# Kernel tuning notes

Hardware: AMD Instinct MI355X
Metric: run time of the kernel (lower is better)

## Reference

```python
import jax, jax.numpy as jnp
import numpy as np

N_NODES = 50000
N_EDGES = 800000
N_FEATS = 64
K_HOPS = 3


def setup_inputs() -> dict:
    key = jax.random.key(0)
    k1, k2, k3 = jax.random.split(key, 3)
    x = jax.random.normal(k1, (N_NODES, N_FEATS), dtype=jnp.float32)
    edge_index = jax.random.randint(k2, (2, N_EDGES), 0, N_NODES, dtype=jnp.int32)
    # SGConv linear: out_channels = 1 (hardcoded in Net)
    W = jax.random.normal(k3, (1, N_FEATS), dtype=jnp.float32) / np.sqrt(N_FEATS)
    b = jnp.zeros((1,), dtype=jnp.float32)
    return {"x": x, "edge_index": edge_index, "W": W, "b": b}


def reference(x, edge_index, W, b):
    # SGConv: X' = (D^-1/2 (A + I) D^-1/2)^K X @ W.T + b
    N = x.shape[0]
    self_loops = jnp.arange(N, dtype=edge_index.dtype)
    row = jnp.concatenate([edge_index[0], self_loops])  # source nodes (x_j)
    col = jnp.concatenate([edge_index[1], self_loops])  # destination nodes
    # gcn_norm: degree computed at destination with unit edge weights
    deg = jax.ops.segment_sum(jnp.ones(row.shape[0], x.dtype), col, num_segments=N)
    dinv = jnp.where(deg > 0, jax.lax.rsqrt(deg), jnp.zeros_like(deg))
    norm = dinv[row] * dinv[col]  # [E + N]
    # K hops of normalized sparse propagation: out[col] += norm * x[row]
    for _ in range(K_HOPS):
        x = jax.ops.segment_sum(norm[:, None] * x[row], col, num_segments=N)
    return x @ W.T + b  # [N, 1]
```

## Files before the change

kernel.cpp:

```cpp
#include <hip/hip_runtime.h>

#define N_NODES 50000
#define N_EDGES 800000
#define N_FEATS 64
#define EB4     (N_EDGES / 4)
#define NBUCK   256
#define BRANGE  196
#define CAPB    4096
#define NTHR    1024
#define CHUNK   ((EB4 + NBUCK - 1) / NBUCK)
#define MAXREC  (CHUNK * 4)

union SmemU {
    struct { unsigned buf[MAXREC]; unsigned adr[MAXREC]; } so;
    unsigned recs_l[CAPB];
};

__device__ __forceinline__ void gbar(unsigned* bar, unsigned target) {
    __syncthreads();
    if (threadIdx.x == 0) {
        __hip_atomic_fetch_add(bar, 1u, __ATOMIC_RELAXED, __HIP_MEMORY_SCOPE_AGENT);
        while (__hip_atomic_load(bar, __ATOMIC_RELAXED, __HIP_MEMORY_SCOPE_AGENT) < target)
            __builtin_amdgcn_s_sleep(2);
    }
    __syncthreads();
}

__device__ __forceinline__ void st_agent(float* p, float v) {
    __hip_atomic_store(p, v, __ATOMIC_RELAXED, __HIP_MEMORY_SCOPE_AGENT);
}
__device__ __forceinline__ void st_agent_u(unsigned* p, unsigned v) {
    __hip_atomic_store(p, v, __ATOMIC_RELAXED, __HIP_MEMORY_SCOPE_AGENT);
}
__device__ __forceinline__ float ld_agent(const float* p) {
    return __hip_atomic_load(p, __ATOMIC_RELAXED, __HIP_MEMORY_SCOPE_AGENT);
}
__device__ __forceinline__ unsigned ld_agent_u(const unsigned* p) {
    return __hip_atomic_load(p, __ATOMIC_RELAXED, __HIP_MEMORY_SCOPE_AGENT);
}
__device__ __forceinline__ unsigned long long ld_agent_u64(const unsigned long long* p) {
    return __hip_atomic_load(p, __ATOMIC_RELAXED, __HIP_MEMORY_SCOPE_AGENT);
}

__global__ void __launch_bounds__(NTHR) k_fused(
    const float* __restrict__ x, const int* __restrict__ ei,
    const float* __restrict__ w, const float* __restrict__ bptr,
    float* __restrict__ out,
    unsigned* __restrict__ bars, int* __restrict__ gcur,
    unsigned* __restrict__ recs, float* __restrict__ z0, float* __restrict__ z1)
{
    __shared__ SmemU u;
    __shared__ int   s_cnt[NBUCK];
    __shared__ int   s_off[NBUCK];
    __shared__ int   s_wsum[4];
    __shared__ int   s_total;
    __shared__ float s_dinv[BRANGE];
    __shared__ float s_z[BRANGE];
    __shared__ float s_acc[BRANGE];

    const int t = threadIdx.x;
    const int blk = blockIdx.x;
    const int* row = ei;
    const int* col = ei + N_EDGES;

    if (t < NBUCK) s_cnt[t] = 0;
    __syncthreads();

    const int g = blk * CHUNK + t;
    const bool valid = (t < CHUNK) && (g < EB4);
    int4 c4, r4;
    int bk0, bk1, bk2, bk3, rk0, rk1, rk2, rk3;
    if (valid) {
        c4 = ((const int4*)col)[g];
        r4 = ((const int4*)row)[g];
        bk0 = c4.x / BRANGE; rk0 = atomicAdd(&s_cnt[bk0], 1);
        bk1 = c4.y / BRANGE; rk1 = atomicAdd(&s_cnt[bk1], 1);
        bk2 = c4.z / BRANGE; rk2 = atomicAdd(&s_cnt[bk2], 1);
        bk3 = c4.w / BRANGE; rk3 = atomicAdd(&s_cnt[bk3], 1);
    }
    __syncthreads();

    if (t < NBUCK) {
        const int lane = t & 63;
        const int cnt = s_cnt[t];
        int val = cnt;
        #pragma unroll
        for (int d = 1; d < 64; d <<= 1) {
            int tmp = __shfl_up(val, d);
            if (lane >= d) val += tmp;
        }
        if (lane == 63) s_wsum[t >> 6] = val;
        s_off[t] = val - cnt;
    }
    __syncthreads();
    if (t < NBUCK) {
        const int w4 = t >> 6;
        int base = 0;
        #pragma unroll
        for (int i = 0; i < 3; i++) if (i < w4) base += s_wsum[i];
        s_off[t] += base;
        const int cnt = s_cnt[t];
        s_cnt[t] = cnt ? atomicAdd(&gcur[t], cnt) : 0;
        if (t == 0) s_total = s_wsum[0] + s_wsum[1] + s_wsum[2] + s_wsum[3];
    }
    __syncthreads();

    if (valid) {
        const int cc[4] = {c4.x, c4.y, c4.z, c4.w};
        const int rr[4] = {r4.x, r4.y, r4.z, r4.w};
        const int bb[4] = {bk0, bk1, bk2, bk3};
        const int kk[4] = {rk0, rk1, rk2, rk3};
        #pragma unroll
        for (int i = 0; i < 4; i++) {
            const int b = bb[i];
            const int p = s_off[b] + kk[i];
            const int slot = s_cnt[b] + kk[i];
            u.so.buf[p] = ((unsigned)(cc[i] - b * BRANGE) << 16) | (unsigned)rr[i];
            u.so.adr[p] = (slot < CAPB) ? (unsigned)(b * CAPB + slot) : 0xFFFFFFFFu;
        }
    }
    __syncthreads();

    const int total = s_total;
    for (int p = t; p < total; p += NTHR) {
        const unsigned a = u.so.adr[p];
        if (a != 0xFFFFFFFFu) st_agent_u(&recs[a], u.so.buf[p]);
    }

    const int ln = t >> 2;
    const int pp = t & 3;
    const int node = blk * BRANGE + ln;
    if (ln < BRANGE && node < N_NODES) {
        const float4* xr = (const float4*)(x + (size_t)node * N_FEATS + pp * 16);
        const float4* wr = (const float4*)(w + pp * 16);
        float a = 0.0f;
        #pragma unroll
        for (int k = 0; k < 4; k++) {
            const float4 v = xr[k];
            const float4 q = wr[k];
            a += v.x * q.x + v.y * q.y + v.z * q.z + v.w * q.w;
        }
        a += __shfl_xor(a, 1);
        a += __shfl_xor(a, 2);
        if (pp == 0) s_z[ln] = a;
    }
    __syncthreads();
    if (t < BRANGE) s_cnt[t] = 0;

    gbar(bars, 1 * NBUCK);

    const int sz = min((int)ld_agent_u((const unsigned*)&gcur[blk]), CAPB);

    const unsigned long long* rb2 =
        (const unsigned long long*)(recs + (size_t)blk * CAPB);
    const int sz2 = sz >> 1;
    for (int e = t; e < sz2; e += NTHR) {
        const unsigned long long v = ld_agent_u64(&rb2[e]);
        const unsigned r0 = (unsigned)v;
        const unsigned r1 = (unsigned)(v >> 32);
        ((unsigned long long*)u.recs_l)[e] = v;
        atomicAdd(&s_cnt[r0 >> 16], 1);
        atomicAdd(&s_cnt[r1 >> 16], 1);
    }
    if (t == 0 && (sz & 1)) {
        const unsigned r = ld_agent_u(&recs[(size_t)blk * CAPB + sz - 1]);
        u.recs_l[sz - 1] = r;
        atomicAdd(&s_cnt[r >> 16], 1);
    }
    __syncthreads();

    if (t < BRANGE) {
        const float d = rsqrtf((float)(s_cnt[t] + 1));
        s_dinv[t] = d;
        const int nd = blk * BRANGE + t;
        if (nd < N_NODES) {
            const float zv = d * s_z[t];
            s_z[t] = zv;
            st_agent(&z0[nd], zv);
        }
    }

    gbar(bars, 2 * NBUCK);

    const float* zin = z0;
    float* zout = z1;
    const int sz4 = sz >> 2;
    #pragma unroll 1
    for (int hop = 0; hop < 3; ++hop) {
        if (t < BRANGE) s_acc[t] = 0.0f;
        __syncthreads();

        const uint4* rl4 = (const uint4*)u.recs_l;
        for (int e = t; e < sz4; e += NTHR) {
            const uint4 r = rl4[e];
            const float v0 = ld_agent(&zin[r.x & 0xFFFFu]);
            const float v1 = ld_agent(&zin[r.y & 0xFFFFu]);
            const float v2 = ld_agent(&zin[r.z & 0xFFFFu]);
            const float v3 = ld_agent(&zin[r.w & 0xFFFFu]);
            atomicAdd(&s_acc[r.x >> 16], v0);
            atomicAdd(&s_acc[r.y >> 16], v1);
            atomicAdd(&s_acc[r.z >> 16], v2);
            atomicAdd(&s_acc[r.w >> 16], v3);
        }
        if (t < (sz & 3)) {
            const unsigned r = u.recs_l[(sz4 << 2) + t];
            atomicAdd(&s_acc[r >> 16], ld_agent(&zin[r & 0xFFFFu]));
        }
        __syncthreads();

        if (t < BRANGE) {
            const int nd = blk * BRANGE + t;
            if (nd < N_NODES) {
                const float d = s_dinv[t];
                const float v = s_z[t] + s_acc[t];
                if (hop == 2) {
                    out[nd] = d * v + bptr[0];
                } else {
                    const float nz = d * d * v;
                    s_z[t] = nz;
                    st_agent(&zout[nd], nz);
                }
            }
        }
        if (hop < 2) {
            gbar(bars, (unsigned)(3 + hop) * NBUCK);
            const float* tmp = zin;
            zin = zout;
            zout = const_cast<float*>(tmp);
        }
    }
}


extern "C" void kernel_launch(void* const* d_in, const int* in_sizes, int n_in,
                              void* d_out, int out_size, void* d_ws, size_t ws_size,
                              hipStream_t stream) {
    const float* x  = (const float*)d_in[0];
    const int*   ei = (const int*)d_in[1];
    const float* W  = (const float*)d_in[2];
    const float* b  = (const float*)d_in[3];
    float* out = (float*)d_out;

    unsigned* bars = (unsigned*)d_ws;
    int*      gcur = (int*)(bars + 64);
    unsigned* recs = (unsigned*)(gcur + NBUCK);
    float*    z0   = (float*)(recs + (size_t)NBUCK * CAPB);
    float*    z1   = z0 + N_NODES;

    hipMemsetAsync(bars, 0, (64 + NBUCK) * sizeof(unsigned), stream);

    k_fused<<<dim3(NBUCK), dim3(NTHR), 0, stream>>>(
        x, ei, W, b, out, bars, gcur, recs, z0, z1);
}
```

Measured before the change: 115.9 us.

## Shard grid barrier counters, triple-buffer z, and use plain cached gather loads

Replaces the single-counter grid barrier with 32 sharded counters that are polled by a warp and summed with shuffles, which cuts atomic contention on one address. It uses three separate z buffers (one per hop) so the gathers can use plain cached loads instead of agent-scope atomic loads. The z arrays get a padded per-block stride, with source indices remapped at record build time. The x·W projection is moved earlier so it overlaps the bucketing, and record loading is unrolled into two loads per thread. The risk is that plain loads of freshly written z values depend on caches staying coherent across the barrier, since each hop writes to a fresh buffer.

```diff
diff --git a/kernel.cpp b/kernel.cpp
--- a/kernel.cpp
+++ b/kernel.cpp
@@ -6,40 +6,72 @@
 #define EB4     (N_EDGES / 4)
 #define NBUCK   256
 #define BRANGE  196
+#define ZSTRIDE 208
 #define CAPB    4096
 #define NTHR    1024
 #define CHUNK   ((EB4 + NBUCK - 1) / NBUCK)
 #define MAXREC  (CHUNK * 4)
+#define BARW    32
 
 union SmemU {
     struct { unsigned buf[MAXREC]; unsigned adr[MAXREC]; } so;
     unsigned recs_l[CAPB];
 };
 
-__device__ __forceinline__ void gbar(unsigned* bar, unsigned target) {
-    __syncthreads();
-    if (threadIdx.x == 0) {
-        __hip_atomic_fetch_add(bar, 1u, __ATOMIC_RELAXED, __HIP_MEMORY_SCOPE_AGENT);
-        while (__hip_atomic_load(bar, __ATOMIC_RELAXED, __HIP_MEMORY_SCOPE_AGENT) < target)
-            __builtin_amdgcn_s_sleep(2);
-    }
-    __syncthreads();
-}
-
 __device__ __forceinline__ void st_agent(float* p, float v) {
     __hip_atomic_store(p, v, __ATOMIC_RELAXED, __HIP_MEMORY_SCOPE_AGENT);
 }
 __device__ __forceinline__ void st_agent_u(unsigned* p, unsigned v) {
     __hip_atomic_store(p, v, __ATOMIC_RELAXED, __HIP_MEMORY_SCOPE_AGENT);
 }
-__device__ __forceinline__ float ld_agent(const float* p) {
-    return __hip_atomic_load(p, __ATOMIC_RELAXED, __HIP_MEMORY_SCOPE_AGENT);
-}
 __device__ __forceinline__ unsigned ld_agent_u(const unsigned* p) {
     return __hip_atomic_load(p, __ATOMIC_RELAXED, __HIP_MEMORY_SCOPE_AGENT);
 }
 __device__ __forceinline__ unsigned long long ld_agent_u64(const unsigned long long* p) {
     return __hip_atomic_load(p, __ATOMIC_RELAXED, __HIP_MEMORY_SCOPE_AGENT);
+}
+
+__device__ __forceinline__ void gbar(unsigned* bars, int k) {
+    __syncthreads();
+    const int t = threadIdx.x;
+    if (t == 0)
+        __hip_atomic_fetch_add(&bars[k * BARW + (blockIdx.x & (BARW - 1))], 1u,
+                               __ATOMIC_RELAXED, __HIP_MEMORY_SCOPE_AGENT);
+    if (t < BARW) {
+        unsigned s;
+        do {
+            __builtin_amdgcn_s_sleep(1);
+            s = __hip_atomic_load(&bars[k * BARW + t],
+                                  __ATOMIC_RELAXED, __HIP_MEMORY_SCOPE_AGENT);
+            #pragma unroll
+            for (int d = 1; d < BARW; d <<= 1)
+                s += (unsigned)__shfl_xor((int)s, d);
+        } while (s < NBUCK);
+    }
+    __syncthreads();
+}
+
+__device__ __forceinline__ void gather(const unsigned* recs_l, int sz,
+                                       const float* __restrict__ zin,
+                                       float* s_acc) {
+    const int t = threadIdx.x;
+    const int sz4 = sz >> 2;
+    const uint4* rl4 = (const uint4*)recs_l;
+    for (int e = t; e < sz4; e += NTHR) {
+        const uint4 r = rl4[e];
+        const float v0 = zin[r.x & 0xFFFFu];
+        const float v1 = zin[r.y & 0xFFFFu];
+        const float v2 = zin[r.z & 0xFFFFu];
+        const float v3 = zin[r.w & 0xFFFFu];
+        atomicAdd(&s_acc[r.x >> 16], v0);
+        atomicAdd(&s_acc[r.y >> 16], v1);
+        atomicAdd(&s_acc[r.z >> 16], v2);
+        atomicAdd(&s_acc[r.w >> 16], v3);
+    }
+    if (t < (sz & 3)) {
+        const unsigned r = recs_l[(sz4 << 2) + t];
+        atomicAdd(&s_acc[r >> 16], zin[r & 0xFFFFu]);
+    }
 }
 
 __global__ void __launch_bounds__(NTHR) k_fused(
@@ -47,7 +79,8 @@
     const float* __restrict__ w, const float* __restrict__ bptr,
     float* __restrict__ out,
     unsigned* __restrict__ bars, int* __restrict__ gcur,
-    unsigned* __restrict__ recs, float* __restrict__ z0, float* __restrict__ z1)
+    unsigned* __restrict__ recs,
+    float* __restrict__ zA, float* __restrict__ zB, float* __restrict__ zC)
 {
     __shared__ SmemU u;
     __shared__ int   s_cnt[NBUCK];
@@ -78,6 +111,23 @@
         bk2 = c4.z / BRANGE; rk2 = atomicAdd(&s_cnt[bk2], 1);
         bk3 = c4.w / BRANGE; rk3 = atomicAdd(&s_cnt[bk3], 1);
     }
+
+    const int ln = t >> 2;
+    const int pp = t & 3;
+    const int node = blk * BRANGE + ln;
+    float mv = 0.0f;
+    if (ln < BRANGE && node < N_NODES) {
+        const float4* xr = (const float4*)(x + (size_t)node * N_FEATS + pp * 16);
+        const float4* wr = (const float4*)(w + pp * 16);
+        #pragma unroll
+        for (int k = 0; k < 4; k++) {
+            const float4 v = xr[k];
+            const float4 q = wr[k];
+            mv += v.x * q.x + v.y * q.y + v.z * q.z + v.w * q.w;
+        }
+        mv += __shfl_xor(mv, 1);
+        mv += __shfl_xor(mv, 2);
+    }
     __syncthreads();
 
     if (t < NBUCK) {
@@ -115,7 +165,9 @@
             const int b = bb[i];
             const int p = s_off[b] + kk[i];
             const int slot = s_cnt[b] + kk[i];
-            u.so.buf[p] = ((unsigned)(cc[i] - b * BRANGE) << 16) | (unsigned)rr[i];
+            const unsigned src = (unsigned)rr[i];
+            const unsigned psrc = src + 12u * (src / (unsigned)BRANGE);
+            u.so.buf[p] = ((unsigned)(cc[i] - b * BRANGE) << 16) | psrc;
             u.so.adr[p] = (slot < CAPB) ? (unsigned)(b * CAPB + slot) : 0xFFFFFFFFu;
         }
     }
@@ -126,46 +178,38 @@
         const unsigned a = u.so.adr[p];
         if (a != 0xFFFFFFFFu) st_agent_u(&recs[a], u.so.buf[p]);
     }
-
-    const int ln = t >> 2;
-    const int pp = t & 3;
-    const int node = blk * BRANGE + ln;
-    if (ln < BRANGE && node < N_NODES) {
-        const float4* xr = (const float4*)(x + (size_t)node * N_FEATS + pp * 16);
-        const float4* wr = (const float4*)(w + pp * 16);
-        float a = 0.0f;
-        #pragma unroll
-        for (int k = 0; k < 4; k++) {
-            const float4 v = xr[k];
-            const float4 q = wr[k];
-            a += v.x * q.x + v.y * q.y + v.z * q.z + v.w * q.w;
-        }
-        a += __shfl_xor(a, 1);
-        a += __shfl_xor(a, 2);
-        if (pp == 0) s_z[ln] = a;
-    }
     __syncthreads();
     if (t < BRANGE) s_cnt[t] = 0;
-
-    gbar(bars, 1 * NBUCK);
+    if (pp == 0 && ln < BRANGE) s_z[ln] = mv;
+
+    gbar(bars, 0);
 
     const int sz = min((int)ld_agent_u((const unsigned*)&gcur[blk]), CAPB);
-
-    const unsigned long long* rb2 =
-        (const unsigned long long*)(recs + (size_t)blk * CAPB);
     const int sz2 = sz >> 1;
-    for (int e = t; e < sz2; e += NTHR) {
-        const unsigned long long v = ld_agent_u64(&rb2[e]);
-        const unsigned r0 = (unsigned)v;
-        const unsigned r1 = (unsigned)(v >> 32);
-        ((unsigned long long*)u.recs_l)[e] = v;
-        atomicAdd(&s_cnt[r0 >> 16], 1);
-        atomicAdd(&s_cnt[r1 >> 16], 1);
-    }
-    if (t == 0 && (sz & 1)) {
-        const unsigned r = ld_agent_u(&recs[(size_t)blk * CAPB + sz - 1]);
-        u.recs_l[sz - 1] = r;
-        atomicAdd(&s_cnt[r >> 16], 1);
+
+    {
+        const unsigned long long* rb2 =
+            (const unsigned long long*)(recs + (size_t)blk * CAPB);
+        const bool e0 = t < sz2;
+        const bool e1 = t + NTHR < sz2;
+        unsigned long long v0 = 0, v1 = 0;
+        if (e0) v0 = ld_agent_u64(&rb2[t]);
+        if (e1) v1 = ld_agent_u64(&rb2[t + NTHR]);
+        if (e0) {
+            ((unsigned long long*)u.recs_l)[t] = v0;
+            atomicAdd(&s_cnt[((unsigned)v0) >> 16], 1);
+            atomicAdd(&s_cnt[((unsigned)(v0 >> 32)) >> 16], 1);
+        }
+        if (e1) {
+            ((unsigned long long*)u.recs_l)[t + NTHR] = v1;
+            atomicAdd(&s_cnt[((unsigned)v1) >> 16], 1);
+            atomicAdd(&s_cnt[((unsigned)(v1 >> 32)) >> 16], 1);
+        }
+        if (t == 0 && (sz & 1)) {
+            const unsigned r = ld_agent_u(&recs[(size_t)blk * CAPB + sz - 1]);
+            u.recs_l[sz - 1] = r;
+            atomicAdd(&s_cnt[r >> 16], 1);
+        }
     }
     __syncthreads();
 
@@ -176,58 +220,50 @@
         if (nd < N_NODES) {
             const float zv = d * s_z[t];
             s_z[t] = zv;
-            st_agent(&z0[nd], zv);
-        }
-    }
-
-    gbar(bars, 2 * NBUCK);
-
-    const float* zin = z0;
-    float* zout = z1;
-    const int sz4 = sz >> 2;
-    #pragma unroll 1
-    for (int hop = 0; hop < 3; ++hop) {
-        if (t < BRANGE) s_acc[t] = 0.0f;
-        __syncthreads();
-
-        const uint4* rl4 = (const uint4*)u.recs_l;
-        for (int e = t; e < sz4; e += NTHR) {
-            const uint4 r = rl4[e];
-            const float v0 = ld_agent(&zin[r.x & 0xFFFFu]);
-            const float v1 = ld_agent(&zin[r.y & 0xFFFFu]);
-            const float v2 = ld_agent(&zin[r.z & 0xFFFFu]);
-            const float v3 = ld_agent(&zin[r.w & 0xFFFFu]);
-            atomicAdd(&s_acc[r.x >> 16], v0);
-            atomicAdd(&s_acc[r.y >> 16], v1);
-            atomicAdd(&s_acc[r.z >> 16], v2);
-            atomicAdd(&s_acc[r.w >> 16], v3);
-        }
-        if (t < (sz & 3)) {
-            const unsigned r = u.recs_l[(sz4 << 2) + t];
-            atomicAdd(&s_acc[r >> 16], ld_agent(&zin[r & 0xFFFFu]));
-        }
-        __syncthreads();
-
-        if (t < BRANGE) {
-            const int nd = blk * BRANGE + t;
-            if (nd < N_NODES) {
-                const float d = s_dinv[t];
-                const float v = s_z[t] + s_acc[t];
-                if (hop == 2) {
-                    out[nd] = d * v + bptr[0];
-                } else {
-                    const float nz = d * d * v;
-                    s_z[t] = nz;
-                    st_agent(&zout[nd], nz);
-                }
-            }
-        }
-        if (hop < 2) {
-            gbar(bars, (unsigned)(3 + hop) * NBUCK);
-            const float* tmp = zin;
-            zin = zout;
-            zout = const_cast<float*>(tmp);
-        }
+            st_agent(&zA[blk * ZSTRIDE + t], zv);
+        }
+    }
+
+    gbar(bars, 1);
+
+    if (t < BRANGE) s_acc[t] = 0.0f;
+    __syncthreads();
+    gather(u.recs_l, sz, zA, s_acc);
+    __syncthreads();
+    if (t < BRANGE) {
+        const int nd = blk * BRANGE + t;
+        if (nd < N_NODES) {
+            const float d = s_dinv[t];
+            const float nz = d * d * (s_z[t] + s_acc[t]);
+            s_z[t] = nz;
+            st_agent(&zB[blk * ZSTRIDE + t], nz);
+        }
+    }
+    gbar(bars, 2);
+
+    if (t < BRANGE) s_acc[t] = 0.0f;
+    __syncthreads();
+    gather(u.recs_l, sz, zB, s_acc);
+    __syncthreads();
+    if (t < BRANGE) {
+        const int nd = blk * BRANGE + t;
+        if (nd < N_NODES) {
+            const float d = s_dinv[t];
+            const float nz = d * d * (s_z[t] + s_acc[t]);
+            s_z[t] = nz;
+            st_agent(&zC[blk * ZSTRIDE + t], nz);
+        }
+    }
+    gbar(bars, 3);
+
+    if (t < BRANGE) s_acc[t] = 0.0f;
+    __syncthreads();
+    gather(u.recs_l, sz, zC, s_acc);
+    __syncthreads();
+    if (t < BRANGE) {
+        const int nd = blk * BRANGE + t;
+        if (nd < N_NODES)
+            out[nd] = s_dinv[t] * (s_z[t] + s_acc[t]) + bptr[0];
     }
 }
 
@@ -242,13 +278,14 @@
     float* out = (float*)d_out;
 
     unsigned* bars = (unsigned*)d_ws;
-    int*      gcur = (int*)(bars + 64);
+    int*      gcur = (int*)(bars + 4 * BARW);
     unsigned* recs = (unsigned*)(gcur + NBUCK);
-    float*    z0   = (float*)(recs + (size_t)NBUCK * CAPB);
-    float*    z1   = z0 + N_NODES;
-
-    hipMemsetAsync(bars, 0, (64 + NBUCK) * sizeof(unsigned), stream);
+    float*    zA   = (float*)(recs + (size_t)NBUCK * CAPB);
+    float*    zB   = zA + (size_t)NBUCK * ZSTRIDE;
+    float*    zC   = zB + (size_t)NBUCK * ZSTRIDE;
+
+    hipMemsetAsync(bars, 0, (4 * BARW + NBUCK) * sizeof(unsigned), stream);
 
     k_fused<<<dim3(NBUCK), dim3(NTHR), 0, stream>>>(
-        x, ei, W, b, out, bars, gcur, recs, z0, z1);
-}
+        x, ei, W, b, out, bars, gcur, recs, zA, zB, zC);
+}
```

After: 112.6 us. 2.8% less time.
